# Performance work log

Measured on AMD Instinct MI355X. Metric: run time of the kernel, lower is better.

Reference implementation:

```python
import jax, jax.numpy as jnp
import numpy as np

NUM_FEATURES = 1_000_000
EMB_DIM = 16
NUM_FIELDS = 39
CIN_SIZES = (200, 200, 200)
DNN_SIZES = (400, 400)


def setup_inputs() -> dict:
    key = jax.random.key(0)
    ks = jax.random.split(key, 16)
    B = 2048
    inp = {}
    inp["feature_ids"] = jax.random.randint(ks[0], (B, NUM_FIELDS), 0, NUM_FEATURES)
    inp["feature_vals"] = jax.random.uniform(ks[1], (B, NUM_FIELDS), dtype=jnp.float32)
    # embeddings (xavier-normal-ish scale)
    inp["emb"] = jax.random.normal(ks[2], (NUM_FEATURES, EMB_DIM), jnp.float32) * 0.02
    inp["bias_emb"] = jax.random.normal(ks[3], (NUM_FEATURES, 1), jnp.float32) * 0.02
    # CIN conv1d (kernel size 1) weights: (out, in)
    field_nums = [NUM_FIELDS]
    for i, size in enumerate(CIN_SIZES):
        cin_in = field_nums[-1] * NUM_FIELDS
        inp[f"cin_W{i}"] = jax.random.normal(ks[4 + i], (size, cin_in), jnp.float32) / np.sqrt(cin_in)
        inp[f"cin_b{i}"] = jnp.zeros((size,), jnp.float32)
        field_nums.append(size // 2 if i != len(CIN_SIZES) - 1 else size)
    # DNN linears: (out, in)
    last = NUM_FIELDS * EMB_DIM
    for i, size in enumerate(DNN_SIZES):
        inp[f"dnn_W{i}"] = jax.random.normal(ks[8 + i], (size, last), jnp.float32) / np.sqrt(last)
        inp[f"dnn_b{i}"] = jnp.zeros((size,), jnp.float32)
        last = size
    hidden_size = sum(CIN_SIZES[:-1]) // 2 + CIN_SIZES[-1]  # 400
    fc_in = hidden_size + DNN_SIZES[-1]
    inp["fc_W"] = jax.random.normal(ks[12], (1, fc_in), jnp.float32) / np.sqrt(fc_in)
    inp["fc_b"] = jnp.zeros((1,), jnp.float32)
    return inp


def _forward(feature_ids, feature_vals, emb, bias_emb,
             cin_W0, cin_b0, cin_W1, cin_b1, cin_W2, cin_b2,
             dnn_W0, dnn_b0, dnn_W1, dnn_b1, fc_W, fc_b):
    B = feature_ids.shape[0]
    inputs = emb[feature_ids] * feature_vals[:, :, None]        # [B, F, D]
    input_biases = bias_emb[feature_ids][..., 0] * feature_vals  # [B, F]

    # CIN
    Ws = (cin_W0, cin_W1, cin_W2)
    bs = (cin_b0, cin_b1, cin_b2)
    h = inputs
    finals = []
    n_layers = len(CIN_SIZES)
    for i in range(n_layers):
        size = CIN_SIZES[i]
        x = jnp.einsum('bhd,bmd->bhmd', h, inputs)              # [B, H, F, D]
        x = x.reshape(B, -1, EMB_DIM)                           # [B, H*F, D]
        x = jnp.einsum('bcd,oc->bod', x, Ws[i]) + bs[i][None, :, None]  # 1x1 conv
        x = jax.nn.relu(x)
        if i != n_layers - 1:
            h, direct = x[:, : size // 2], x[:, size // 2:]
        else:
            direct = x
        finals.append(direct)
    cin_result = jnp.sum(jnp.concatenate(finals, axis=1), axis=-1)  # [B, hidden]

    # DNN
    d = inputs.reshape(B, -1)
    d = jax.nn.relu(d @ dnn_W0.T + dnn_b0)
    d = jax.nn.relu(d @ dnn_W1.T + dnn_b1)

    out = (jnp.concatenate((cin_result, d), axis=1) @ fc_W.T + fc_b)[:, 0]
    return out + jnp.sum(input_biases, axis=1)                  # [B]


def reference(feature_ids, feature_vals, emb, bias_emb,
              cin_W0, cin_b0, cin_W1, cin_b1, cin_W2, cin_b2,
              dnn_W0, dnn_b0, dnn_W1, dnn_b1, fc_W, fc_b):
    return _forward(feature_ids, feature_vals, emb, bias_emb,
                    cin_W0, cin_b0, cin_W1, cin_b1, cin_W2, cin_b2,
                    dnn_W0, dnn_b0, dnn_W1, dnn_b1, fc_W, fc_b)
```

## Files before the change

### kernel.cpp

```cpp
#include <hip/hip_runtime.h>

#define B 2048
#define NF 39
#define D 16

typedef __bf16 bf16x8 __attribute__((ext_vector_type(8)));
typedef float f32x4 __attribute__((ext_vector_type(4)));

__device__ __forceinline__ void lds_barrier() {
  asm volatile("s_waitcnt lgkmcnt(0)" ::: "memory");
  __builtin_amdgcn_s_barrier();
}

__global__ __launch_bounds__(256) void gather_kernel(
    const int* __restrict__ fid, const float* __restrict__ fval,
    const float* __restrict__ emb, const float* __restrict__ bias_emb,
    float* __restrict__ inputs, float* __restrict__ biassum) {
  int b = blockIdx.x;
  __shared__ int ids[NF];
  __shared__ float vals[NF];
  int t = threadIdx.x;
  if (t < NF) { ids[t] = fid[b * NF + t]; vals[t] = fval[b * NF + t]; }
  __syncthreads();
  for (int i = t; i < NF * D; i += 256) {
    int f = i >> 4, d = i & 15;
    inputs[b * NF * D + i] = emb[(long)ids[f] * D + d] * vals[f];
  }
  if (t < 64) {
    float pb = (t < NF) ? bias_emb[ids[t]] * vals[t] : 0.f;
#pragma unroll
    for (int m = 32; m >= 1; m >>= 1) pb += __shfl_xor(pb, m);
    if (t == 0) biassum[b] = pb;
  }
}

__global__ void prep_w_kernel(const float* __restrict__ W, __bf16* __restrict__ Wg,
                              int Hreal, int nch) {
  int idx = blockIdx.x * 256 + threadIdx.x;
  int total = nch * 13 * 64;
  if (idx >= total) return;
  int l = idx & 63;
  int mt = (idx >> 6) % 13;
  int c = idx / (13 * 64);
  int o = mt * 16 + (l & 15);
  int kb = c * 32 + ((l >> 4) << 3);
  int rowlen = Hreal * 39;
  bf16x8 v;
#pragma unroll
  for (int j = 0; j < 8; ++j) {
    int k = kb + j;
    int h = k / 40;
    int m = k - h * 40;
    float val = 0.f;
    if (o < 200 && h < Hreal && m < 39) val = W[(long)o * rowlen + h * 39 + m];
    v[j] = (__bf16)val;
  }
  *reinterpret_cast<bf16x8*>(Wg + (long)idx * 8) = v;
}

__global__ void prep_dnn_w(const float* __restrict__ W, __bf16* __restrict__ Wd,
                           int IN, int nch) {
  int idx = blockIdx.x * 256 + threadIdx.x;
  int total = nch * 25 * 64;
  if (idx >= total) return;
  int l = idx & 63;
  int tt = (idx >> 6) % 25;
  int c = idx / (25 * 64);
  int o = tt * 16 + (l & 15);
  int kb = c * 32 + ((l >> 4) << 3);
  bf16x8 v;
#pragma unroll
  for (int j = 0; j < 8; ++j) {
    int k = kb + j;
    v[j] = (k < IN) ? (__bf16)W[(long)o * IN + k] : (__bf16)0.f;
  }
  *reinterpret_cast<bf16x8*>(Wd + (long)idx * 8) = v;
}

__device__ __forceinline__ void form_x(const float* Hs, const float* Zs,
                                       __bf16* xbuf, int k0, int col) {
  int h = (int)((unsigned)k0 / 40u);
  int m0 = k0 - h * 40;
  float hv = Hs[h * 64 + col];
  const float4* zp = reinterpret_cast<const float4*>(Zs + col * 44 + m0);
  float4 za = zp[0], zb = zp[1];
  bf16x8 xv;
  xv[0] = (__bf16)(hv * za.x); xv[1] = (__bf16)(hv * za.y);
  xv[2] = (__bf16)(hv * za.z); xv[3] = (__bf16)(hv * za.w);
  xv[4] = (__bf16)(hv * zb.x); xv[5] = (__bf16)(hv * zb.y);
  xv[6] = (__bf16)(hv * zb.z); xv[7] = (__bf16)(hv * zb.w);
  int g = (k0 >> 3) & 7;
  *reinterpret_cast<bf16x8*>(
      reinterpret_cast<char*>(xbuf) + col * 128 + ((g * 16) ^ ((col & 7) << 4))) = xv;
}

template <int NW, int NST, int SPLIT>
__device__ __forceinline__ void cin_layer(
    float* Hs, const float* Zs, __bf16* Xs,
    const __bf16* __restrict__ Wg, const float* __restrict__ bias,
    float* __restrict__ cin_out, int col_offset, int bbase, int t) {
  constexpr int TLO = (13 * NW) >> 2;
  const int l = t & 63;
  const int q = l >> 4, dd = l & 15;

  f32x4 acc[13] = {};
  bf16x8 wf[8], wfn[8];
  const __bf16* wp = Wg + l * 8 + TLO * 512;
#pragma unroll
  for (int i = 0; i < 4; ++i)
#pragma unroll
    for (int hf = 0; hf < 2; ++hf)
      wf[i * 2 + hf] = *reinterpret_cast<const bf16x8*>(wp + hf * 6656 + i * 512);

  form_x(Hs, Zs, Xs, NW * 8, l);
  form_x(Hs, Zs, Xs, (NW + 4) * 8, l);
  lds_barrier();

  for (int s = 0; s < NST; ++s) {
    __bf16* xcur = Xs + (s & 1) * 4096;
    __bf16* xnxt = Xs + ((s + 1) & 1) * 4096;
    const bool more = (s + 1 < NST);
    if (more) {
      const __bf16* wq = wp + 13312;
#pragma unroll
      for (int i = 0; i < 4; ++i)
#pragma unroll
        for (int hf = 0; hf < 2; ++hf)
          wfn[i * 2 + hf] =
              *reinterpret_cast<const bf16x8*>(wq + hf * 6656 + i * 512);
    }
    bf16x8 bfr[4][2];
#pragma unroll
    for (int f = 0; f < 4; ++f)
#pragma unroll
      for (int hf = 0; hf < 2; ++hf) {
        int col = f * 16 + dd;
        int g = q + hf * 4;
        bfr[f][hf] = *reinterpret_cast<const bf16x8*>(
            reinterpret_cast<const char*>(xcur) + col * 128 +
            ((g * 16) ^ ((col & 7) << 4)));
      }
    if (more) {
      form_x(Hs, Zs, xnxt, (s + 1) * 64 + NW * 8, l);
      form_x(Hs, Zs, xnxt, (s + 1) * 64 + (NW + 4) * 8, l);
    }
    __builtin_amdgcn_s_setprio(1);
#pragma unroll
    for (int i = 0; i < 13; ++i) {
      const int p = 13 * NW + i;
      const int ti = (p >> 2) - TLO;
      const int f = p & 3;
      acc[i] = __builtin_amdgcn_mfma_f32_16x16x32_bf16(wf[ti * 2 + 0], bfr[f][0],
                                                       acc[i], 0, 0, 0);
      acc[i] = __builtin_amdgcn_mfma_f32_16x16x32_bf16(wf[ti * 2 + 1], bfr[f][1],
                                                       acc[i], 0, 0, 0);
    }
    __builtin_amdgcn_s_setprio(0);
    lds_barrier();
    if (more) {
#pragma unroll
      for (int i = 0; i < 8; ++i) wf[i] = wfn[i];
      wp += 13312;
    }
  }

#pragma unroll
  for (int i = 0; i < 13; ++i) {
    const int p = 13 * NW + i;
    const int tt = p >> 2, f = p & 3;
    const int b = bbase + f;
#pragma unroll
    for (int r = 0; r < 4; ++r) {
      int o = tt * 16 + q * 4 + r;
      if (o < 200) {
        float x = fmaxf(acc[i][r] + bias[o], 0.f);
        if (SPLIT && o < 100) {
          Hs[o * 64 + f * 16 + dd] = x;
        } else {
          x += __shfl_xor(x, 1);
          x += __shfl_xor(x, 2);
          x += __shfl_xor(x, 4);
          x += __shfl_xor(x, 8);
          if (dd == 0) cin_out[b * 400 + col_offset + o - (SPLIT ? 100 : 0)] = x;
        }
      }
    }
  }
  lds_barrier();
}

template <int NW>
__device__ __forceinline__ void cin_all(
    float* Hs, const float* Zs, __bf16* Xs, const __bf16* Wg0,
    const __bf16* Wg1, const __bf16* Wg2, const float* cb0, const float* cb1,
    const float* cb2, float* cinres, int bbase, int t) {
  cin_layer<NW, 25, 1>(Hs, Zs, Xs, Wg0, cb0, cinres, 0, bbase, t);
  cin_layer<NW, 63, 1>(Hs, Zs, Xs, Wg1, cb1, cinres, 100, bbase, t);
  cin_layer<NW, 63, 0>(Hs, Zs, Xs, Wg2, cb2, cinres, 200, bbase, t);
}

__global__ __launch_bounds__(256, 2) void cin_fused(
    const float* __restrict__ Zin, const __bf16* __restrict__ Wg0,
    const __bf16* __restrict__ Wg1, const __bf16* __restrict__ Wg2,
    const float* __restrict__ cb0, const float* __restrict__ cb1,
    const float* __restrict__ cb2, float* __restrict__ cinres) {
  __shared__ float Hs[101 * 64];
  __shared__ float Zs[64 * 44];
  __shared__ __bf16 Xs[2 * 64 * 64];
  const int t = threadIdx.x;
  const int bbase = blockIdx.x * 4;

  for (int i = t; i < 64 * 40; i += 256) {
    int col = i / 40, m = i - (i / 40) * 40;
    int b = bbase + (col >> 4), d = col & 15;
    Zs[col * 44 + m] = (m < NF) ? Zin[((long)b * NF + m) * 16 + d] : 0.f;
  }
  for (int i = t; i < 41 * 64; i += 256) {
    int h = i >> 6, col = i & 63;
    int b = bbase + (col >> 4), d = col & 15;
    Hs[i] = (h < NF) ? Zin[((long)b * NF + h) * 16 + d] : 0.f;
  }
  if (t < 64) Hs[100 * 64 + t] = 0.f;
  __syncthreads();

  const int w = t >> 6;
  if (w == 0) cin_all<0>(Hs, Zs, Xs, Wg0, Wg1, Wg2, cb0, cb1, cb2, cinres, bbase, t);
  else if (w == 1) cin_all<1>(Hs, Zs, Xs, Wg0, Wg1, Wg2, cb0, cb1, cb2, cinres, bbase, t);
  else if (w == 2) cin_all<2>(Hs, Zs, Xs, Wg0, Wg1, Wg2, cb0, cb1, cb2, cinres, bbase, t);
  else cin_all<3>(Hs, Zs, Xs, Wg0, Wg1, Wg2, cb0, cb1, cb2, cinres, bbase, t);
}

template <int IN>
__device__ __forceinline__ void dnn_stage_load(const float* __restrict__ x,
                                               int bg, int c, int t,
                                               float4& a, float4& b2) {
  int b = t >> 2, kb = t & 3;
  int k0 = c * 32 + kb * 8;
  if (k0 < IN) {
    const float4* p =
        reinterpret_cast<const float4*>(x + (long)(bg * 64 + b) * IN + k0);
    a = p[0];
    b2 = p[1];
  } else {
    a = make_float4(0.f, 0.f, 0.f, 0.f);
    b2 = make_float4(0.f, 0.f, 0.f, 0.f);
  }
}

__device__ __forceinline__ void dnn_stage_write(__bf16* Xs, int t, float4 a,
                                                float4 b2) {
  int b = t >> 2, kb = t & 3;
  bf16x8 v;
  v[0] = (__bf16)a.x;  v[1] = (__bf16)a.y;  v[2] = (__bf16)a.z;  v[3] = (__bf16)a.w;
  v[4] = (__bf16)b2.x; v[5] = (__bf16)b2.y; v[6] = (__bf16)b2.z; v[7] = (__bf16)b2.w;
  *reinterpret_cast<bf16x8*>(Xs + ((kb * 64 + b) << 3)) = v;
}

template <int W, int TG, int IN, int NCH>
__device__ __forceinline__ void dnn_core(
    const float* __restrict__ x, const __bf16* __restrict__ Wd,
    const float* __restrict__ bias, float* __restrict__ out, __bf16* Xs,
    int bg, int t) {
  constexpr int NT = (TG == 3) ? 7 : 6;
  constexpr int TGB = TG * 6;
  constexpr int PLO = NT * W;
  constexpr int TLO = PLO >> 2;
  constexpr int TN = ((PLO + NT - 1) >> 2) - TLO + 1;
  const int l = t & 63;
  const int q = l >> 4, dd = l & 15;
  const __bf16* wl = Wd + l * 8;

  f32x4 acc[NT] = {};
  bf16x8 wf[TN], wfn[TN];
#pragma unroll
  for (int i = 0; i < TN; ++i)
    wf[i] = *reinterpret_cast<const bf16x8*>(wl + (long)((TGB + TLO + i) * 64) * 8);

  float4 ra, rb;
  dnn_stage_load<IN>(x, bg, 0, t, ra, rb);
  dnn_stage_write(Xs, t, ra, rb);
  lds_barrier();

  for (int c = 0; c < NCH; ++c) {
    __bf16* cur = Xs + (c & 1) * 2048;
    __bf16* nxt = Xs + ((c + 1) & 1) * 2048;
    const bool more = (c + 1 < NCH);
    if (more) {
      dnn_stage_load<IN>(x, bg, c + 1, t, ra, rb);
#pragma unroll
      for (int i = 0; i < TN; ++i)
        wfn[i] = *reinterpret_cast<const bf16x8*>(
            wl + (long)(((c + 1) * 25 + TGB + TLO + i) * 64) * 8);
    }
    bf16x8 bfr[4];
#pragma unroll
    for (int f = 0; f < 4; ++f)
      bfr[f] = *reinterpret_cast<const bf16x8*>(cur + ((q * 64 + f * 16 + dd) << 3));
    __builtin_amdgcn_s_setprio(1);
#pragma unroll
    for (int i = 0; i < NT; ++i) {
      const int p = PLO + i;
      acc[i] = __builtin_amdgcn_mfma_f32_16x16x32_bf16(wf[(p >> 2) - TLO],
                                                       bfr[p & 3], acc[i], 0, 0, 0);
    }
    __builtin_amdgcn_s_setprio(0);
    if (more) dnn_stage_write(nxt, t, ra, rb);
    lds_barrier();
    if (more) {
#pragma unroll
      for (int i = 0; i < TN; ++i) wf[i] = wfn[i];
    }
  }

#pragma unroll
  for (int i = 0; i < NT; ++i) {
    const int p = PLO + i;
    const int gt = TGB + (p >> 2);
    const int f = p & 3;
    const int b = bg * 64 + f * 16 + dd;
#pragma unroll
    for (int r = 0; r < 4; ++r) {
      int o = gt * 16 + q * 4 + r;
      out[(long)b * 400 + o] = fmaxf(acc[i][r] + bias[o], 0.f);
    }
  }
}

template <int IN, int NCH>
__global__ __launch_bounds__(256) void dnn_mfma(
    const float* __restrict__ x, const __bf16* __restrict__ Wd,
    const float* __restrict__ bias, float* __restrict__ out) {
  __shared__ __bf16 Xs[2 * 4 * 64 * 8];
  const int blk = blockIdx.x;
  const int bg = blk >> 2, tg = blk & 3;
  const int t = threadIdx.x;
  const int w = t >> 6;
#define DNN_DISPATCH(TGV)                                                     \
  if (w == 0) dnn_core<0, TGV, IN, NCH>(x, Wd, bias, out, Xs, bg, t);         \
  else if (w == 1) dnn_core<1, TGV, IN, NCH>(x, Wd, bias, out, Xs, bg, t);    \
  else if (w == 2) dnn_core<2, TGV, IN, NCH>(x, Wd, bias, out, Xs, bg, t);    \
  else dnn_core<3, TGV, IN, NCH>(x, Wd, bias, out, Xs, bg, t);
  if (tg == 0) { DNN_DISPATCH(0) }
  else if (tg == 1) { DNN_DISPATCH(1) }
  else if (tg == 2) { DNN_DISPATCH(2) }
  else { DNN_DISPATCH(3) }
#undef DNN_DISPATCH
}

__global__ __launch_bounds__(256) void final_kernel(
    const float* __restrict__ cin, const float* __restrict__ d1,
    const float* __restrict__ fcW, const float* __restrict__ fcb,
    const float* __restrict__ biassum, float* __restrict__ out) {
  int b = blockIdx.x, t = threadIdx.x;
  float p = 0.f;
  for (int i = t; i < 800; i += 256) {
    float v = (i < 400) ? cin[b * 400 + i] : d1[b * 400 + (i - 400)];
    p += v * fcW[i];
  }
#pragma unroll
  for (int m = 32; m >= 1; m >>= 1) p += __shfl_xor(p, m);
  __shared__ float red[4];
  if ((t & 63) == 0) red[t >> 6] = p;
  __syncthreads();
  if (t == 0) out[b] = red[0] + red[1] + red[2] + red[3] + fcb[0] + biassum[b];
}

extern "C" void kernel_launch(void* const* d_in, const int* in_sizes, int n_in,
                              void* d_out, int out_size, void* d_ws,
                              size_t ws_size, hipStream_t stream) {
  (void)in_sizes; (void)n_in; (void)out_size; (void)ws_size;
  const int* fid = (const int*)d_in[0];
  const float* fval = (const float*)d_in[1];
  const float* emb = (const float*)d_in[2];
  const float* bias_emb = (const float*)d_in[3];
  const float* cW0 = (const float*)d_in[4];
  const float* cb0 = (const float*)d_in[5];
  const float* cW1 = (const float*)d_in[6];
  const float* cb1 = (const float*)d_in[7];
  const float* cW2 = (const float*)d_in[8];
  const float* cb2 = (const float*)d_in[9];
  const float* dW0 = (const float*)d_in[10];
  const float* db0 = (const float*)d_in[11];
  const float* dW1 = (const float*)d_in[12];
  const float* db1 = (const float*)d_in[13];
  const float* fcW = (const float*)d_in[14];
  const float* fcb = (const float*)d_in[15];
  float* out = (float*)d_out;

  float* ws = (float*)d_ws;
  float* inputs = ws;  ws += B * NF * D;
  float* biassum = ws; ws += B;
  float* cinres = ws;  ws += B * 400;
  float* dd0 = ws;     ws += B * 400;
  float* dd1 = ws;     ws += B * 400;
  __bf16* Wg0 = (__bf16*)ws; ws += (50 * 13 * 64 * 8) / 2;
  __bf16* Wg1 = (__bf16*)ws; ws += (126 * 13 * 64 * 8) / 2;
  __bf16* Wg2 = (__bf16*)ws; ws += (126 * 13 * 64 * 8) / 2;
  __bf16* Wd0 = (__bf16*)ws; ws += (20 * 25 * 64 * 8) / 2;
  __bf16* Wd1 = (__bf16*)ws; ws += (13 * 25 * 64 * 8) / 2;

  gather_kernel<<<B, 256, 0, stream>>>(fid, fval, emb, bias_emb, inputs, biassum);

  prep_w_kernel<<<(50 * 13 * 64 + 255) / 256, 256, 0, stream>>>(cW0, Wg0, 39, 50);
  prep_w_kernel<<<(126 * 13 * 64 + 255) / 256, 256, 0, stream>>>(cW1, Wg1, 100, 126);
  prep_w_kernel<<<(126 * 13 * 64 + 255) / 256, 256, 0, stream>>>(cW2, Wg2, 100, 126);
  prep_dnn_w<<<(20 * 25 * 64 + 255) / 256, 256, 0, stream>>>(dW0, Wd0, 624, 20);
  prep_dnn_w<<<(13 * 25 * 64 + 255) / 256, 256, 0, stream>>>(dW1, Wd1, 400, 13);

  cin_fused<<<B / 4, 256, 0, stream>>>(inputs, Wg0, Wg1, Wg2, cb0, cb1, cb2, cinres);

  dnn_mfma<624, 20><<<128, 256, 0, stream>>>(inputs, Wd0, db0, dd0);
  dnn_mfma<400, 13><<<128, 256, 0, stream>>>(dd0, Wd1, db1, dd1);

  final_kernel<<<B, 256, 0, stream>>>(cinres, dd1, fcW, fcb, biassum, out);
}
```

Before: 212.7 us.

## Split CIN K-reduction across two wave groups and merge weight-prep launches

Doubles the CIN block to 512 threads. Each of the eight waves handles half of every 64-wide K chunk, with group G taking 32-element halves, so per-wave MFMA work and register-held weight fragments are halved. Partial accumulators are then reduced through LDS in four serialized barrier rounds before the bias, ReLU and output step. The five weight-preparation kernels are fused into one launch to cut launch overhead. The cost is extra barriers and LDS traffic per layer, and a risk of lower occupancy from the 512-thread, 4-block launch bound.

```diff
diff --git a/kernel.cpp b/kernel.cpp
--- a/kernel.cpp
+++ b/kernel.cpp
@@ -34,11 +34,9 @@
   }
 }
 
-__global__ void prep_w_kernel(const float* __restrict__ W, __bf16* __restrict__ Wg,
-                              int Hreal, int nch) {
-  int idx = blockIdx.x * 256 + threadIdx.x;
-  int total = nch * 13 * 64;
-  if (idx >= total) return;
+__device__ __forceinline__ void prep_cin_one(const float* __restrict__ W,
+                                             __bf16* __restrict__ Wg,
+                                             int Hreal, int idx) {
   int l = idx & 63;
   int mt = (idx >> 6) % 13;
   int c = idx / (13 * 64);
@@ -58,11 +56,9 @@
   *reinterpret_cast<bf16x8*>(Wg + (long)idx * 8) = v;
 }
 
-__global__ void prep_dnn_w(const float* __restrict__ W, __bf16* __restrict__ Wd,
-                           int IN, int nch) {
-  int idx = blockIdx.x * 256 + threadIdx.x;
-  int total = nch * 25 * 64;
-  if (idx >= total) return;
+__device__ __forceinline__ void prep_dnn_one(const float* __restrict__ W,
+                                             __bf16* __restrict__ Wd,
+                                             int IN, int idx) {
   int l = idx & 63;
   int tt = (idx >> 6) % 25;
   int c = idx / (25 * 64);
@@ -75,6 +71,29 @@
     v[j] = (k < IN) ? (__bf16)W[(long)o * IN + k] : (__bf16)0.f;
   }
   *reinterpret_cast<bf16x8*>(Wd + (long)idx * 8) = v;
+}
+
+#define PREP_T0 (50 * 13 * 64)
+#define PREP_T12 (126 * 13 * 64)
+#define PREP_T3 (20 * 25 * 64)
+#define PREP_T4 (13 * 25 * 64)
+#define PREP_TOTAL (PREP_T0 + 2 * PREP_T12 + PREP_T3 + PREP_T4)
+
+__global__ void prep_all(const float* __restrict__ cW0, const float* __restrict__ cW1,
+                         const float* __restrict__ cW2, const float* __restrict__ dW0,
+                         const float* __restrict__ dW1, __bf16* __restrict__ Wg0,
+                         __bf16* __restrict__ Wg1, __bf16* __restrict__ Wg2,
+                         __bf16* __restrict__ Wd0, __bf16* __restrict__ Wd1) {
+  int idx = blockIdx.x * 256 + threadIdx.x;
+  if (idx < PREP_T0) { prep_cin_one(cW0, Wg0, 39, idx); return; }
+  idx -= PREP_T0;
+  if (idx < PREP_T12) { prep_cin_one(cW1, Wg1, 100, idx); return; }
+  idx -= PREP_T12;
+  if (idx < PREP_T12) { prep_cin_one(cW2, Wg2, 100, idx); return; }
+  idx -= PREP_T12;
+  if (idx < PREP_T3) { prep_dnn_one(dW0, Wd0, 624, idx); return; }
+  idx -= PREP_T3;
+  if (idx < PREP_T4) prep_dnn_one(dW1, Wd1, 400, idx);
 }
 
 __device__ __forceinline__ void form_x(const float* Hs, const float* Zs,
@@ -94,112 +113,112 @@
       reinterpret_cast<char*>(xbuf) + col * 128 + ((g * 16) ^ ((col & 7) << 4))) = xv;
 }
 
-template <int NW, int NST, int SPLIT>
+template <int SUB, int G, int NST, int SPLIT>
 __device__ __forceinline__ void cin_layer(
     float* Hs, const float* Zs, __bf16* Xs,
     const __bf16* __restrict__ Wg, const float* __restrict__ bias,
     float* __restrict__ cin_out, int col_offset, int bbase, int t) {
-  constexpr int TLO = (13 * NW) >> 2;
+  constexpr int TLO = (13 * SUB) >> 2;
+  constexpr int W8 = SUB + 4 * G;
   const int l = t & 63;
   const int q = l >> 4, dd = l & 15;
+  const __bf16* wl = Wg + l * 8;
 
   f32x4 acc[13] = {};
-  bf16x8 wf[8], wfn[8];
-  const __bf16* wp = Wg + l * 8 + TLO * 512;
+  bf16x8 wf[4], wfn[4];
 #pragma unroll
   for (int i = 0; i < 4; ++i)
-#pragma unroll
-    for (int hf = 0; hf < 2; ++hf)
-      wf[i * 2 + hf] = *reinterpret_cast<const bf16x8*>(wp + hf * 6656 + i * 512);
-
-  form_x(Hs, Zs, Xs, NW * 8, l);
-  form_x(Hs, Zs, Xs, (NW + 4) * 8, l);
+    wf[i] = *reinterpret_cast<const bf16x8*>(wl + (long)((G * 13 + TLO + i) * 64) * 8);
+
+  form_x(Hs, Zs, Xs, W8 * 8, l);
   lds_barrier();
 
   for (int s = 0; s < NST; ++s) {
     __bf16* xcur = Xs + (s & 1) * 4096;
     __bf16* xnxt = Xs + ((s + 1) & 1) * 4096;
+    const int c = 2 * s + G;
     const bool more = (s + 1 < NST);
     if (more) {
-      const __bf16* wq = wp + 13312;
 #pragma unroll
       for (int i = 0; i < 4; ++i)
-#pragma unroll
-        for (int hf = 0; hf < 2; ++hf)
-          wfn[i * 2 + hf] =
-              *reinterpret_cast<const bf16x8*>(wq + hf * 6656 + i * 512);
-    }
-    bf16x8 bfr[4][2];
-#pragma unroll
-    for (int f = 0; f < 4; ++f)
-#pragma unroll
-      for (int hf = 0; hf < 2; ++hf) {
-        int col = f * 16 + dd;
-        int g = q + hf * 4;
-        bfr[f][hf] = *reinterpret_cast<const bf16x8*>(
-            reinterpret_cast<const char*>(xcur) + col * 128 +
-            ((g * 16) ^ ((col & 7) << 4)));
-      }
-    if (more) {
-      form_x(Hs, Zs, xnxt, (s + 1) * 64 + NW * 8, l);
-      form_x(Hs, Zs, xnxt, (s + 1) * 64 + (NW + 4) * 8, l);
-    }
+        wfn[i] = *reinterpret_cast<const bf16x8*>(
+            wl + (long)(((c + 2) * 13 + TLO + i) * 64) * 8);
+    }
+    bf16x8 bfr[4];
+#pragma unroll
+    for (int f = 0; f < 4; ++f) {
+      int col = f * 16 + dd;
+      int kg = q + 4 * G;
+      bfr[f] = *reinterpret_cast<const bf16x8*>(
+          reinterpret_cast<const char*>(xcur) + col * 128 +
+          ((kg * 16) ^ ((col & 7) << 4)));
+    }
+    if (more) form_x(Hs, Zs, xnxt, (s + 1) * 64 + W8 * 8, l);
     __builtin_amdgcn_s_setprio(1);
 #pragma unroll
     for (int i = 0; i < 13; ++i) {
-      const int p = 13 * NW + i;
+      const int p = 13 * SUB + i;
       const int ti = (p >> 2) - TLO;
       const int f = p & 3;
-      acc[i] = __builtin_amdgcn_mfma_f32_16x16x32_bf16(wf[ti * 2 + 0], bfr[f][0],
-                                                       acc[i], 0, 0, 0);
-      acc[i] = __builtin_amdgcn_mfma_f32_16x16x32_bf16(wf[ti * 2 + 1], bfr[f][1],
-                                                       acc[i], 0, 0, 0);
+      acc[i] = __builtin_amdgcn_mfma_f32_16x16x32_bf16(wf[ti], bfr[f], acc[i], 0, 0, 0);
     }
     __builtin_amdgcn_s_setprio(0);
     lds_barrier();
     if (more) {
 #pragma unroll
-      for (int i = 0; i < 8; ++i) wf[i] = wfn[i];
-      wp += 13312;
-    }
-  }
-
-#pragma unroll
-  for (int i = 0; i < 13; ++i) {
-    const int p = 13 * NW + i;
-    const int tt = p >> 2, f = p & 3;
-    const int b = bbase + f;
-#pragma unroll
-    for (int r = 0; r < 4; ++r) {
-      int o = tt * 16 + q * 4 + r;
-      if (o < 200) {
-        float x = fmaxf(acc[i][r] + bias[o], 0.f);
-        if (SPLIT && o < 100) {
-          Hs[o * 64 + f * 16 + dd] = x;
-        } else {
-          x += __shfl_xor(x, 1);
-          x += __shfl_xor(x, 2);
-          x += __shfl_xor(x, 4);
-          x += __shfl_xor(x, 8);
-          if (dd == 0) cin_out[b * 400 + col_offset + o - (SPLIT ? 100 : 0)] = x;
+      for (int i = 0; i < 4; ++i) wf[i] = wfn[i];
+    }
+  }
+
+  f32x4* Xred = reinterpret_cast<f32x4*>(Xs);
+#pragma unroll
+  for (int r = 0; r < 4; ++r) {
+    if (G == 1 && SUB == r) {
+#pragma unroll
+      for (int i = 0; i < 13; ++i) Xred[i * 64 + l] = acc[i];
+    }
+    lds_barrier();
+    if (G == 0 && SUB == r) {
+#pragma unroll
+      for (int i = 0; i < 13; ++i) {
+        f32x4 a = acc[i];
+        f32x4 bpart = Xred[i * 64 + l];
+        const int p = 13 * SUB + i;
+        const int tt = p >> 2, f = p & 3;
+        const int b = bbase + f;
+#pragma unroll
+        for (int rr = 0; rr < 4; ++rr) {
+          int o = tt * 16 + q * 4 + rr;
+          if (o < 200) {
+            float x = fmaxf(a[rr] + bpart[rr] + bias[o], 0.f);
+            if (SPLIT && o < 100) {
+              Hs[o * 64 + f * 16 + dd] = x;
+            } else {
+              x += __shfl_xor(x, 1);
+              x += __shfl_xor(x, 2);
+              x += __shfl_xor(x, 4);
+              x += __shfl_xor(x, 8);
+              if (dd == 0) cin_out[b * 400 + col_offset + o - (SPLIT ? 100 : 0)] = x;
+            }
+          }
         }
       }
     }
-  }
-  lds_barrier();
-}
-
-template <int NW>
+    lds_barrier();
+  }
+}
+
+template <int SUB, int G>
 __device__ __forceinline__ void cin_all(
     float* Hs, const float* Zs, __bf16* Xs, const __bf16* Wg0,
     const __bf16* Wg1, const __bf16* Wg2, const float* cb0, const float* cb1,
     const float* cb2, float* cinres, int bbase, int t) {
-  cin_layer<NW, 25, 1>(Hs, Zs, Xs, Wg0, cb0, cinres, 0, bbase, t);
-  cin_layer<NW, 63, 1>(Hs, Zs, Xs, Wg1, cb1, cinres, 100, bbase, t);
-  cin_layer<NW, 63, 0>(Hs, Zs, Xs, Wg2, cb2, cinres, 200, bbase, t);
-}
-
-__global__ __launch_bounds__(256, 2) void cin_fused(
+  cin_layer<SUB, G, 25, 1>(Hs, Zs, Xs, Wg0, cb0, cinres, 0, bbase, t);
+  cin_layer<SUB, G, 63, 1>(Hs, Zs, Xs, Wg1, cb1, cinres, 100, bbase, t);
+  cin_layer<SUB, G, 63, 0>(Hs, Zs, Xs, Wg2, cb2, cinres, 200, bbase, t);
+}
+
+__global__ __launch_bounds__(512, 4) void cin_fused(
     const float* __restrict__ Zin, const __bf16* __restrict__ Wg0,
     const __bf16* __restrict__ Wg1, const __bf16* __restrict__ Wg2,
     const float* __restrict__ cb0, const float* __restrict__ cb1,
@@ -210,12 +229,12 @@
   const int t = threadIdx.x;
   const int bbase = blockIdx.x * 4;
 
-  for (int i = t; i < 64 * 40; i += 256) {
+  for (int i = t; i < 64 * 40; i += 512) {
     int col = i / 40, m = i - (i / 40) * 40;
     int b = bbase + (col >> 4), d = col & 15;
     Zs[col * 44 + m] = (m < NF) ? Zin[((long)b * NF + m) * 16 + d] : 0.f;
   }
-  for (int i = t; i < 41 * 64; i += 256) {
+  for (int i = t; i < 41 * 64; i += 512) {
     int h = i >> 6, col = i & 63;
     int b = bbase + (col >> 4), d = col & 15;
     Hs[i] = (h < NF) ? Zin[((long)b * NF + h) * 16 + d] : 0.f;
@@ -224,10 +243,16 @@
   __syncthreads();
 
   const int w = t >> 6;
-  if (w == 0) cin_all<0>(Hs, Zs, Xs, Wg0, Wg1, Wg2, cb0, cb1, cb2, cinres, bbase, t);
-  else if (w == 1) cin_all<1>(Hs, Zs, Xs, Wg0, Wg1, Wg2, cb0, cb1, cb2, cinres, bbase, t);
-  else if (w == 2) cin_all<2>(Hs, Zs, Xs, Wg0, Wg1, Wg2, cb0, cb1, cb2, cinres, bbase, t);
-  else cin_all<3>(Hs, Zs, Xs, Wg0, Wg1, Wg2, cb0, cb1, cb2, cinres, bbase, t);
+  switch (w) {
+    case 0: cin_all<0, 0>(Hs, Zs, Xs, Wg0, Wg1, Wg2, cb0, cb1, cb2, cinres, bbase, t); break;
+    case 1: cin_all<1, 0>(Hs, Zs, Xs, Wg0, Wg1, Wg2, cb0, cb1, cb2, cinres, bbase, t); break;
+    case 2: cin_all<2, 0>(Hs, Zs, Xs, Wg0, Wg1, Wg2, cb0, cb1, cb2, cinres, bbase, t); break;
+    case 3: cin_all<3, 0>(Hs, Zs, Xs, Wg0, Wg1, Wg2, cb0, cb1, cb2, cinres, bbase, t); break;
+    case 4: cin_all<0, 1>(Hs, Zs, Xs, Wg0, Wg1, Wg2, cb0, cb1, cb2, cinres, bbase, t); break;
+    case 5: cin_all<1, 1>(Hs, Zs, Xs, Wg0, Wg1, Wg2, cb0, cb1, cb2, cinres, bbase, t); break;
+    case 6: cin_all<2, 1>(Hs, Zs, Xs, Wg0, Wg1, Wg2, cb0, cb1, cb2, cinres, bbase, t); break;
+    default: cin_all<3, 1>(Hs, Zs, Xs, Wg0, Wg1, Wg2, cb0, cb1, cb2, cinres, bbase, t); break;
+  }
 }
 
 template <int IN>
@@ -401,13 +426,10 @@
 
   gather_kernel<<<B, 256, 0, stream>>>(fid, fval, emb, bias_emb, inputs, biassum);
 
-  prep_w_kernel<<<(50 * 13 * 64 + 255) / 256, 256, 0, stream>>>(cW0, Wg0, 39, 50);
-  prep_w_kernel<<<(126 * 13 * 64 + 255) / 256, 256, 0, stream>>>(cW1, Wg1, 100, 126);
-  prep_w_kernel<<<(126 * 13 * 64 + 255) / 256, 256, 0, stream>>>(cW2, Wg2, 100, 126);
-  prep_dnn_w<<<(20 * 25 * 64 + 255) / 256, 256, 0, stream>>>(dW0, Wd0, 624, 20);
-  prep_dnn_w<<<(13 * 25 * 64 + 255) / 256, 256, 0, stream>>>(dW1, Wd1, 400, 13);
-
-  cin_fused<<<B / 4, 256, 0, stream>>>(inputs, Wg0, Wg1, Wg2, cb0, cb1, cb2, cinres);
+  prep_all<<<(PREP_TOTAL + 255) / 256, 256, 0, stream>>>(
+      cW0, cW1, cW2, dW0, dW1, Wg0, Wg1, Wg2, Wd0, Wd1);
+
+  cin_fused<<<B / 4, 512, 0, stream>>>(inputs, Wg0, Wg1, Wg2, cb0, cb1, cb2, cinres);
 
   dnn_mfma<624, 20><<<128, 256, 0, stream>>>(inputs, Wd0, db0, dd0);
   dnn_mfma<400, 13><<<128, 256, 0, stream>>>(dd0, Wd1, db1, dd1);
```

New measurement: 255.6 us. 1.2x slower.
